# Performance work log

Hardware: AMD Instinct MI355X
Metric: run time of the kernel (lower is better)

The kernel has to match this reference:

```python
import jax, jax.numpy as jnp
import numpy as np

NEG_INF = -1e9  # finite mask value; exp underflows to exactly 0 in fp32


def setup_inputs() -> dict:
    key = jax.random.key(0)
    k1, k2 = jax.random.split(key)
    B, T, D = 16, 2048, 512
    x = jax.random.normal(k1, (B, T, D), dtype=jnp.float32)
    w = jax.random.normal(k2, (D, 1), dtype=jnp.float32) * (D ** -0.5)
    b = jnp.zeros((1,), dtype=jnp.float32)
    return {"x": x, "w": w, "b": b}


def reference(x, w, b):
    # x: [B,T,D]; Dense(1) scores shared across all output steps
    B, T, D = x.shape
    s = jnp.squeeze(x @ w, -1) + b[0]              # [B,T] per-position scalar score
    # output step t (t>=1) attends over strict prefix j < t.
    # row r = t-1 in [0, T-1): valid j <= r  -> lower-triangular mask [T-1, T]
    mask = jnp.tril(jnp.ones((T - 1, T), dtype=bool))
    logits = jnp.where(mask[None], s[:, None, :], NEG_INF)  # [B,T-1,T]
    attn = jax.nn.softmax(logits, axis=-1)                  # [B,T-1,T]
    ctx = jnp.einsum('brj,bjd->brd', attn, x)               # [B,T-1,D]
    # t == 0: passthrough of encoder output at step 0
    return jnp.concatenate([x[:, :1, :], ctx], axis=1)      # [B,T,D]
```

## Files before the change

### kernel.cpp

```cpp
#include <hip/hip_runtime.h>
#include <math.h>

#define B  16
#define T  2048
#define D  512
#define NS 64
#define L  (T / NS)
#define D4 (D / 4)

__device__ __forceinline__ void fma4(float4& a, float s, const float4& v) {
    a.x = fmaf(s, v.x, a.x); a.y = fmaf(s, v.y, a.y);
    a.z = fmaf(s, v.z, a.z); a.w = fmaf(s, v.w, a.w);
}

__global__ __launch_bounds__(256) void seg_kernel(const float* __restrict__ x,
                                                  const float* __restrict__ w,
                                                  const float* __restrict__ bias,
                                                  float* __restrict__ p_loc,
                                                  float* __restrict__ m_out,
                                                  float* __restrict__ q_out,
                                                  float* __restrict__ V) {
    int b = blockIdx.x / NS, k = blockIdx.x % NS;
    int t0 = k * L;
    int tid = threadIdx.x, lane = tid & 63, wv = tid >> 6;
    const float4* x4 = (const float4*)x + ((size_t)b * T + t0) * D4;
    const float4* w4 = (const float4*)w;
    float4 w0 = w4[lane], w1 = w4[lane + 64];

    float4 xr0[8], xr1[8];
    float dots[8];
#pragma unroll
    for (int r = 0; r < 8; ++r) {
        int j = wv * 8 + r;
        xr0[r] = x4[(size_t)j * D4 + lane];
        xr1[r] = x4[(size_t)j * D4 + lane + 64];
        dots[r] = xr0[r].x * w0.x + xr0[r].y * w0.y + xr0[r].z * w0.z + xr0[r].w * w0.w +
                  xr1[r].x * w1.x + xr1[r].y * w1.y + xr1[r].z * w1.z + xr1[r].w * w1.w;
    }

    __shared__ float s_sh[L], e_sh[L];
    __shared__ float accbuf[4][D];

#pragma unroll
    for (int r = 0; r < 8; ++r) {
        float d = dots[r];
#pragma unroll
        for (int off = 32; off > 0; off >>= 1) d += __shfl_xor(d, off);
        if (lane == 0) s_sh[wv * 8 + r] = d + bias[0];
    }
    __syncthreads();

    float mk = -1e30f;
#pragma unroll
    for (int j = 0; j < L; ++j) mk = fmaxf(mk, s_sh[j]);

    float4 a0 = {0.f, 0.f, 0.f, 0.f}, a1 = {0.f, 0.f, 0.f, 0.f};
#pragma unroll
    for (int r = 0; r < 8; ++r) {
        float e = __expf(s_sh[wv * 8 + r] - mk);
        if (lane == 0) e_sh[wv * 8 + r] = e;
        fma4(a0, e, xr0[r]); fma4(a1, e, xr1[r]);
    }
    ((float4*)accbuf[wv])[lane]      = a0;
    ((float4*)accbuf[wv])[lane + 64] = a1;
    __syncthreads();

    if (tid < 128) {
        float4 s0 = ((float4*)accbuf[0])[tid];
        float4 s1 = ((float4*)accbuf[1])[tid];
        float4 s2 = ((float4*)accbuf[2])[tid];
        float4 s3 = ((float4*)accbuf[3])[tid];
        float4 r;
        r.x = (s0.x + s1.x) + (s2.x + s3.x);
        r.y = (s0.y + s1.y) + (s2.y + s3.y);
        r.z = (s0.z + s1.z) + (s2.z + s3.z);
        r.w = (s0.w + s1.w) + (s2.w + s3.w);
        ((float4*)V)[((size_t)b * NS + k) * D4 + tid] = r;
    }
    if (tid < L) p_loc[(size_t)b * T + t0 + tid] = e_sh[tid];
    if (tid == 0) {
        m_out[b * NS + k] = mk;
        float q = 0.f;
#pragma unroll
        for (int j = 0; j < L; ++j) q += e_sh[j];
        q_out[b * NS + k] = q;
    }
}

__global__ __launch_bounds__(256) void out_kernel(const float* __restrict__ x,
                                                  const float* __restrict__ p_loc,
                                                  const float* __restrict__ m_g,
                                                  const float* __restrict__ q_g,
                                                  const float* __restrict__ V,
                                                  float* __restrict__ out) {
    const int blk = blockIdx.x;
    const int b = blk >> 6, k = blk & (NS - 1);
    const int t0 = k * L;
    const int tid = threadIdx.x, lane = tid & 63, wv = tid >> 6;

    const float4* x4 = (const float4*)x + ((size_t)b * T + t0) * D4;
    float4 xr0[8], xr1[8];
#pragma unroll
    for (int r = 0; r < 8; ++r) {
        const int j = wv * 8 + r;
        xr0[r] = x4[(size_t)j * D4 + lane];
        xr1[r] = x4[(size_t)j * D4 + lane + 64];
    }

    __shared__ float accbuf[4][D];
    __shared__ float sc_sh[NS];
    __shared__ float wl[L], il[L];

    const float m_i = m_g[b * NS + lane];
    const float q_i = q_g[b * NS + lane];
    float M = m_i;
#pragma unroll
    for (int off = 32; off > 0; off >>= 1) M = fmaxf(M, __shfl_xor(M, off));
    const float sc_i = __expf(m_i - M);
    const float qp = sc_i * q_i;
    float incl = qp;
#pragma unroll
    for (int off = 1; off < 64; off <<= 1) {
        const float t = __shfl_up(incl, off);
        if (lane >= off) incl += t;
    }
    const float Qexcl = __shfl(incl - qp, k);
    const float sck   = __shfl(sc_i, k);
    if (wv == 0) sc_sh[lane] = sc_i;
    __syncthreads();

    float4 s0 = {0.f, 0.f, 0.f, 0.f}, s1 = {0.f, 0.f, 0.f, 0.f};
    for (int kp = wv; kp < k; kp += 4) {
        const float sc = sc_sh[kp];
        const float4* Vp = (const float4*)V + ((size_t)b * NS + kp) * D4;
        fma4(s0, sc, Vp[lane]);
        fma4(s1, sc, Vp[lane + 64]);
    }
    ((float4*)accbuf[wv])[lane]      = s0;
    ((float4*)accbuf[wv])[lane + 64] = s1;

    if (wv == 0) {
        const float e_j = (lane < L) ? p_loc[(size_t)b * T + t0 + lane] : 0.f;
        float ce = e_j;
#pragma unroll
        for (int off = 1; off < 32; off <<= 1) {
            const float t = __shfl_up(ce, off);
            if (lane >= off) ce += t;
        }
        if (lane < L) {
            wl[lane] = sck * e_j;
            il[lane] = 1.0f / fmaf(sck, ce, Qexcl);
        }
    }
    __syncthreads();

    float4 seed0, seed1;
    {
        const float4 c0 = ((float4*)accbuf[0])[lane];
        const float4 c1 = ((float4*)accbuf[1])[lane];
        const float4 c2 = ((float4*)accbuf[2])[lane];
        const float4 c3 = ((float4*)accbuf[3])[lane];
        seed0.x = (c0.x + c1.x) + (c2.x + c3.x);
        seed0.y = (c0.y + c1.y) + (c2.y + c3.y);
        seed0.z = (c0.z + c1.z) + (c2.z + c3.z);
        seed0.w = (c0.w + c1.w) + (c2.w + c3.w);
        const float4 d0 = ((float4*)accbuf[0])[lane + 64];
        const float4 d1 = ((float4*)accbuf[1])[lane + 64];
        const float4 d2 = ((float4*)accbuf[2])[lane + 64];
        const float4 d3 = ((float4*)accbuf[3])[lane + 64];
        seed1.x = (d0.x + d1.x) + (d2.x + d3.x);
        seed1.y = (d0.y + d1.y) + (d2.y + d3.y);
        seed1.z = (d0.z + d1.z) + (d2.z + d3.z);
        seed1.w = (d0.w + d1.w) + (d2.w + d3.w);
    }

    float wcr[8], ilr[8];
    float4 t0v = {0.f, 0.f, 0.f, 0.f}, t1v = {0.f, 0.f, 0.f, 0.f};
#pragma unroll
    for (int r = 0; r < 8; ++r) {
        wcr[r] = wl[wv * 8 + r];
        ilr[r] = il[wv * 8 + r];
        fma4(t0v, wcr[r], xr0[r]); fma4(t1v, wcr[r], xr1[r]);
    }
    __syncthreads();
    ((float4*)accbuf[wv])[lane]      = t0v;
    ((float4*)accbuf[wv])[lane + 64] = t1v;
    __syncthreads();

    float4 p0 = seed0, p1 = seed1;
    for (int w2 = 0; w2 < wv; ++w2) {
        const float4 c0 = ((float4*)accbuf[w2])[lane];
        const float4 c1 = ((float4*)accbuf[w2])[lane + 64];
        p0.x += c0.x; p0.y += c0.y; p0.z += c0.z; p0.w += c0.w;
        p1.x += c1.x; p1.y += c1.y; p1.z += c1.z; p1.w += c1.w;
    }

    float4* outb = (float4*)out + (size_t)b * T * D4;
    if (k == 0 && wv == 0) {
        outb[lane]      = xr0[0];
        outb[lane + 64] = xr1[0];
    }
#pragma unroll
    for (int r = 0; r < 8; ++r) {
        fma4(p0, wcr[r], xr0[r]); fma4(p1, wcr[r], xr1[r]);
        const int t = t0 + wv * 8 + r;
        if (t < T - 1) {
            const float idn = ilr[r];
            float4 o0, o1;
            o0.x = p0.x * idn; o0.y = p0.y * idn; o0.z = p0.z * idn; o0.w = p0.w * idn;
            o1.x = p1.x * idn; o1.y = p1.y * idn; o1.z = p1.z * idn; o1.w = p1.w * idn;
            outb[(size_t)(t + 1) * D4 + lane]      = o0;
            outb[(size_t)(t + 1) * D4 + lane + 64] = o1;
        }
    }
}

extern "C" void kernel_launch(void* const* d_in, const int* in_sizes, int n_in,
                              void* d_out, int out_size, void* d_ws, size_t ws_size,
                              hipStream_t stream) {
    const float* x    = (const float*)d_in[0];
    const float* w    = (const float*)d_in[1];
    const float* bias = (const float*)d_in[2];
    float* out = (float*)d_out;

    float* p_loc = (float*)d_ws;
    float* m     = p_loc + (size_t)B * T;
    float* q     = m     + (size_t)B * NS;
    float* V     = q     + (size_t)B * NS;

    seg_kernel<<<B * NS, 256, 0, stream>>>(x, w, bias, p_loc, m, q, V);
    out_kernel<<<B * NS, 256, 0, stream>>>(x, p_loc, m, q, V, out);
}
```

Measured before the change: 41.06 us.

## Fuse segment and output kernels into single-pass decoupled-lookback kernel

Merges the two kernels into one. Each block takes a virtual block id from an atomic counter, publishes its segment max, sum and weighted vector V, then spin-waits on per-segment flags of earlier segments in the same batch before computing its outputs. This removes the second launch, the second read of x, and the p_loc round trip through global memory. In exchange it adds a memset, atomic spin-waits with a serial dependency chain across segments, and a 4-blocks-per-CU launch bound.

After: 110.1 us. 2.68x slower.

```diff
diff --git a/kernel.cpp b/kernel.cpp
--- a/kernel.cpp
+++ b/kernel.cpp
@@ -13,25 +13,30 @@
     a.z = fmaf(s, v.z, a.z); a.w = fmaf(s, v.w, a.w);
 }
 
-__global__ __launch_bounds__(256) void seg_kernel(const float* __restrict__ x,
-                                                  const float* __restrict__ w,
-                                                  const float* __restrict__ bias,
-                                                  float* __restrict__ p_loc,
-                                                  float* __restrict__ m_out,
-                                                  float* __restrict__ q_out,
-                                                  float* __restrict__ V) {
-    int b = blockIdx.x / NS, k = blockIdx.x % NS;
-    int t0 = k * L;
-    int tid = threadIdx.x, lane = tid & 63, wv = tid >> 6;
+__global__ __launch_bounds__(256, 4) void fused_lookback(
+        const float* __restrict__ x, const float* __restrict__ w,
+        const float* __restrict__ bias,
+        int* __restrict__ counter, int* __restrict__ flags,
+        float* __restrict__ m_g, float* __restrict__ q_g,
+        float* __restrict__ V, float* __restrict__ out) {
+    const int tid = threadIdx.x, lane = tid & 63, wv = tid >> 6;
+
+    __shared__ int vb_sh;
+    if (tid == 0) vb_sh = atomicAdd(counter, 1);
+    __syncthreads();
+    const int blk = vb_sh;
+    const int b = blk >> 6, k = blk & (NS - 1);
+    const int t0 = k * L;
+
     const float4* x4 = (const float4*)x + ((size_t)b * T + t0) * D4;
     const float4* w4 = (const float4*)w;
-    float4 w0 = w4[lane], w1 = w4[lane + 64];
+    const float4 w0 = w4[lane], w1 = w4[lane + 64];
 
     float4 xr0[8], xr1[8];
     float dots[8];
 #pragma unroll
     for (int r = 0; r < 8; ++r) {
-        int j = wv * 8 + r;
+        const int j = wv * 8 + r;
         xr0[r] = x4[(size_t)j * D4 + lane];
         xr1[r] = x4[(size_t)j * D4 + lane + 64];
         dots[r] = xr0[r].x * w0.x + xr0[r].y * w0.y + xr0[r].z * w0.z + xr0[r].w * w0.w +
@@ -40,6 +45,8 @@
 
     __shared__ float s_sh[L], e_sh[L];
     __shared__ float accbuf[4][D];
+    __shared__ float sc_sh[NS];
+    __shared__ float wl[L], il[L];
 
 #pragma unroll
     for (int r = 0; r < 8; ++r) {
@@ -57,7 +64,7 @@
     float4 a0 = {0.f, 0.f, 0.f, 0.f}, a1 = {0.f, 0.f, 0.f, 0.f};
 #pragma unroll
     for (int r = 0; r < 8; ++r) {
-        float e = __expf(s_sh[wv * 8 + r] - mk);
+        const float e = __expf(s_sh[wv * 8 + r] - mk);
         if (lane == 0) e_sh[wv * 8 + r] = e;
         fma4(a0, e, xr0[r]); fma4(a1, e, xr1[r]);
     }
@@ -66,67 +73,60 @@
     __syncthreads();
 
     if (tid < 128) {
-        float4 s0 = ((float4*)accbuf[0])[tid];
-        float4 s1 = ((float4*)accbuf[1])[tid];
-        float4 s2 = ((float4*)accbuf[2])[tid];
-        float4 s3 = ((float4*)accbuf[3])[tid];
-        float4 r;
-        r.x = (s0.x + s1.x) + (s2.x + s3.x);
-        r.y = (s0.y + s1.y) + (s2.y + s3.y);
-        r.z = (s0.z + s1.z) + (s2.z + s3.z);
-        r.w = (s0.w + s1.w) + (s2.w + s3.w);
-        ((float4*)V)[((size_t)b * NS + k) * D4 + tid] = r;
-    }
-    if (tid < L) p_loc[(size_t)b * T + t0 + tid] = e_sh[tid];
+        const float4 r0 = ((float4*)accbuf[0])[tid];
+        const float4 r1 = ((float4*)accbuf[1])[tid];
+        const float4 r2 = ((float4*)accbuf[2])[tid];
+        const float4 r3 = ((float4*)accbuf[3])[tid];
+        float4 rr;
+        rr.x = (r0.x + r1.x) + (r2.x + r3.x);
+        rr.y = (r0.y + r1.y) + (r2.y + r3.y);
+        rr.z = (r0.z + r1.z) + (r2.z + r3.z);
+        rr.w = (r0.w + r1.w) + (r2.w + r3.w);
+        ((float4*)V)[(size_t)blk * D4 + tid] = rr;
+    }
     if (tid == 0) {
-        m_out[b * NS + k] = mk;
+        m_g[blk] = mk;
         float q = 0.f;
 #pragma unroll
         for (int j = 0; j < L; ++j) q += e_sh[j];
-        q_out[b * NS + k] = q;
-    }
-}
-
-__global__ __launch_bounds__(256) void out_kernel(const float* __restrict__ x,
-                                                  const float* __restrict__ p_loc,
-                                                  const float* __restrict__ m_g,
-                                                  const float* __restrict__ q_g,
-                                                  const float* __restrict__ V,
-                                                  float* __restrict__ out) {
-    const int blk = blockIdx.x;
-    const int b = blk >> 6, k = blk & (NS - 1);
-    const int t0 = k * L;
-    const int tid = threadIdx.x, lane = tid & 63, wv = tid >> 6;
-
-    const float4* x4 = (const float4*)x + ((size_t)b * T + t0) * D4;
-    float4 xr0[8], xr1[8];
-#pragma unroll
-    for (int r = 0; r < 8; ++r) {
-        const int j = wv * 8 + r;
-        xr0[r] = x4[(size_t)j * D4 + lane];
-        xr1[r] = x4[(size_t)j * D4 + lane + 64];
-    }
-
-    __shared__ float accbuf[4][D];
-    __shared__ float sc_sh[NS];
-    __shared__ float wl[L], il[L];
-
-    const float m_i = m_g[b * NS + lane];
-    const float q_i = q_g[b * NS + lane];
-    float M = m_i;
-#pragma unroll
-    for (int off = 32; off > 0; off >>= 1) M = fmaxf(M, __shfl_xor(M, off));
-    const float sc_i = __expf(m_i - M);
-    const float qp = sc_i * q_i;
-    float incl = qp;
-#pragma unroll
-    for (int off = 1; off < 64; off <<= 1) {
-        const float t = __shfl_up(incl, off);
-        if (lane >= off) incl += t;
-    }
-    const float Qexcl = __shfl(incl - qp, k);
-    const float sck   = __shfl(sc_i, k);
-    if (wv == 0) sc_sh[lane] = sc_i;
+        q_g[blk] = q;
+    }
+    __syncthreads();
+    if (tid == 0) {
+        __threadfence();
+        __hip_atomic_store(&flags[blk], 1, __ATOMIC_RELEASE, __HIP_MEMORY_SCOPE_AGENT);
+    }
+
+    if (wv == 0) {
+        float mj = -1e30f, qj = 0.f;
+        if (lane < k) {
+            while (__hip_atomic_load(&flags[b * NS + lane], __ATOMIC_ACQUIRE,
+                                     __HIP_MEMORY_SCOPE_AGENT) == 0)
+                __builtin_amdgcn_s_sleep(2);
+            mj = m_g[b * NS + lane];
+            qj = q_g[b * NS + lane];
+        }
+        float REF = fmaxf(mk, mj);
+#pragma unroll
+        for (int off = 32; off > 0; off >>= 1) REF = fmaxf(REF, __shfl_xor(REF, off));
+        const float scj = (lane < k) ? __expf(mj - REF) : 0.f;
+        sc_sh[lane] = scj;
+        float qp = scj * qj;
+#pragma unroll
+        for (int off = 32; off > 0; off >>= 1) qp += __shfl_xor(qp, off);
+        const float sck = __expf(mk - REF);
+        const float e_j = (lane < L) ? e_sh[lane] : 0.f;
+        float ce = e_j;
+#pragma unroll
+        for (int off = 1; off < 32; off <<= 1) {
+            const float t = __shfl_up(ce, off);
+            if (lane >= off) ce += t;
+        }
+        if (lane < L) {
+            wl[lane] = sck * e_j;
+            il[lane] = 1.0f / fmaf(sck, ce, qp);
+        }
+    }
     __syncthreads();
 
     float4 s0 = {0.f, 0.f, 0.f, 0.f}, s1 = {0.f, 0.f, 0.f, 0.f};
@@ -138,20 +138,6 @@
     }
     ((float4*)accbuf[wv])[lane]      = s0;
     ((float4*)accbuf[wv])[lane + 64] = s1;
-
-    if (wv == 0) {
-        const float e_j = (lane < L) ? p_loc[(size_t)b * T + t0 + lane] : 0.f;
-        float ce = e_j;
-#pragma unroll
-        for (int off = 1; off < 32; off <<= 1) {
-            const float t = __shfl_up(ce, off);
-            if (lane >= off) ce += t;
-        }
-        if (lane < L) {
-            wl[lane] = sck * e_j;
-            il[lane] = 1.0f / fmaf(sck, ce, Qexcl);
-        }
-    }
     __syncthreads();
 
     float4 seed0, seed1;
@@ -223,11 +209,13 @@
     const float* bias = (const float*)d_in[2];
     float* out = (float*)d_out;
 
-    float* p_loc = (float*)d_ws;
-    float* m     = p_loc + (size_t)B * T;
-    float* q     = m     + (size_t)B * NS;
-    float* V     = q     + (size_t)B * NS;
-
-    seg_kernel<<<B * NS, 256, 0, stream>>>(x, w, bias, p_loc, m, q, V);
-    out_kernel<<<B * NS, 256, 0, stream>>>(x, p_loc, m, q, V, out);
+    int*   counter = (int*)d_ws;
+    int*   flags   = counter + 64;
+    float* m_g     = (float*)((char*)d_ws + 8192);
+    float* q_g     = m_g + (size_t)B * NS;
+    float* V       = q_g + (size_t)B * NS;
+
+    hipMemsetAsync(d_ws, 0, 8192, stream);
+    fused_lookback<<<B * NS, 256, 0, stream>>>(x, w, bias, counter, flags,
+                                               m_g, q_g, V, out);
 }
```

## Write unnormalized local prefix in first kernel, rescale output in second

Applied to the files above, without the earlier changes.

Moves the intra-segment prefix accumulation over x into the first kernel, which now writes unnormalized partial outputs directly to out along with local cumulative denominators. The second kernel no longer reads x; instead it reads back out, adds the cross-segment seed and rescales. This removes the re-read of x and the per-row FMAs in the second pass, but adds a full extra write and read of the output buffer.

After: 49.19 us. 19.8% more time.

```diff
diff --git a/kernel.cpp b/kernel.cpp
--- a/kernel.cpp
+++ b/kernel.cpp
@@ -5,33 +5,33 @@
 #define T  2048
 #define D  512
 #define NS 64
-#define L  (T / NS)
-#define D4 (D / 4)
+#define L  32
+#define D4 128
 
 __device__ __forceinline__ void fma4(float4& a, float s, const float4& v) {
     a.x = fmaf(s, v.x, a.x); a.y = fmaf(s, v.y, a.y);
     a.z = fmaf(s, v.z, a.z); a.w = fmaf(s, v.w, a.w);
 }
 
-__global__ __launch_bounds__(256) void seg_kernel(const float* __restrict__ x,
-                                                  const float* __restrict__ w,
-                                                  const float* __restrict__ bias,
-                                                  float* __restrict__ p_loc,
-                                                  float* __restrict__ m_out,
-                                                  float* __restrict__ q_out,
-                                                  float* __restrict__ V) {
-    int b = blockIdx.x / NS, k = blockIdx.x % NS;
-    int t0 = k * L;
-    int tid = threadIdx.x, lane = tid & 63, wv = tid >> 6;
+__global__ __launch_bounds__(256) void seg_scan_kernel(
+        const float* __restrict__ x, const float* __restrict__ w,
+        const float* __restrict__ bias,
+        float* __restrict__ m_g, float* __restrict__ q_g,
+        float* __restrict__ V, float* __restrict__ denloc,
+        float* __restrict__ out) {
+    const int b = blockIdx.x >> 6, k = blockIdx.x & (NS - 1);
+    const int t0 = k * L;
+    const int tid = threadIdx.x, lane = tid & 63, wv = tid >> 6;
+
     const float4* x4 = (const float4*)x + ((size_t)b * T + t0) * D4;
     const float4* w4 = (const float4*)w;
-    float4 w0 = w4[lane], w1 = w4[lane + 64];
+    const float4 w0 = w4[lane], w1 = w4[lane + 64];
 
     float4 xr0[8], xr1[8];
     float dots[8];
 #pragma unroll
     for (int r = 0; r < 8; ++r) {
-        int j = wv * 8 + r;
+        const int j = wv * 8 + r;
         xr0[r] = x4[(size_t)j * D4 + lane];
         xr1[r] = x4[(size_t)j * D4 + lane + 64];
         dots[r] = xr0[r].x * w0.x + xr0[r].y * w0.y + xr0[r].z * w0.z + xr0[r].w * w0.w +
@@ -54,62 +54,94 @@
 #pragma unroll
     for (int j = 0; j < L; ++j) mk = fmaxf(mk, s_sh[j]);
 
-    float4 a0 = {0.f, 0.f, 0.f, 0.f}, a1 = {0.f, 0.f, 0.f, 0.f};
-#pragma unroll
-    for (int r = 0; r < 8; ++r) {
-        float e = __expf(s_sh[wv * 8 + r] - mk);
-        if (lane == 0) e_sh[wv * 8 + r] = e;
-        fma4(a0, e, xr0[r]); fma4(a1, e, xr1[r]);
-    }
-    ((float4*)accbuf[wv])[lane]      = a0;
-    ((float4*)accbuf[wv])[lane + 64] = a1;
+    if (wv == 0) {
+        const float e = (lane < L) ? __expf(s_sh[lane] - mk) : 0.f;
+        if (lane < L) e_sh[lane] = e;
+        float q = e;
+#pragma unroll
+        for (int off = 32; off > 0; off >>= 1) q += __shfl_xor(q, off);
+        float ce = e;
+#pragma unroll
+        for (int off = 1; off < 32; off <<= 1) {
+            const float t = __shfl_up(ce, off);
+            if (lane >= off) ce += t;
+        }
+        if (lane < L) denloc[(size_t)b * T + t0 + lane] = ce;
+        if (lane == 0) { m_g[b * NS + k] = mk; q_g[b * NS + k] = q; }
+    }
+    __syncthreads();
+
+    float er[8];
+    float4 t0v = {0.f, 0.f, 0.f, 0.f}, t1v = {0.f, 0.f, 0.f, 0.f};
+#pragma unroll
+    for (int r = 0; r < 8; ++r) {
+        er[r] = e_sh[wv * 8 + r];
+        fma4(t0v, er[r], xr0[r]); fma4(t1v, er[r], xr1[r]);
+    }
+    ((float4*)accbuf[wv])[lane]      = t0v;
+    ((float4*)accbuf[wv])[lane + 64] = t1v;
     __syncthreads();
 
     if (tid < 128) {
-        float4 s0 = ((float4*)accbuf[0])[tid];
-        float4 s1 = ((float4*)accbuf[1])[tid];
-        float4 s2 = ((float4*)accbuf[2])[tid];
-        float4 s3 = ((float4*)accbuf[3])[tid];
-        float4 r;
-        r.x = (s0.x + s1.x) + (s2.x + s3.x);
-        r.y = (s0.y + s1.y) + (s2.y + s3.y);
-        r.z = (s0.z + s1.z) + (s2.z + s3.z);
-        r.w = (s0.w + s1.w) + (s2.w + s3.w);
-        ((float4*)V)[((size_t)b * NS + k) * D4 + tid] = r;
-    }
-    if (tid < L) p_loc[(size_t)b * T + t0 + tid] = e_sh[tid];
-    if (tid == 0) {
-        m_out[b * NS + k] = mk;
-        float q = 0.f;
-#pragma unroll
-        for (int j = 0; j < L; ++j) q += e_sh[j];
-        q_out[b * NS + k] = q;
-    }
-}
-
-__global__ __launch_bounds__(256) void out_kernel(const float* __restrict__ x,
-                                                  const float* __restrict__ p_loc,
-                                                  const float* __restrict__ m_g,
-                                                  const float* __restrict__ q_g,
-                                                  const float* __restrict__ V,
-                                                  float* __restrict__ out) {
-    const int blk = blockIdx.x;
-    const int b = blk >> 6, k = blk & (NS - 1);
+        const float4 r0 = ((float4*)accbuf[0])[tid];
+        const float4 r1 = ((float4*)accbuf[1])[tid];
+        const float4 r2 = ((float4*)accbuf[2])[tid];
+        const float4 r3 = ((float4*)accbuf[3])[tid];
+        float4 rr;
+        rr.x = (r0.x + r1.x) + (r2.x + r3.x);
+        rr.y = (r0.y + r1.y) + (r2.y + r3.y);
+        rr.z = (r0.z + r1.z) + (r2.z + r3.z);
+        rr.w = (r0.w + r1.w) + (r2.w + r3.w);
+        ((float4*)V)[((size_t)b * NS + k) * D4 + tid] = rr;
+    }
+
+    float4 p0 = {0.f, 0.f, 0.f, 0.f}, p1 = {0.f, 0.f, 0.f, 0.f};
+    for (int w2 = 0; w2 < wv; ++w2) {
+        const float4 c0 = ((float4*)accbuf[w2])[lane];
+        const float4 c1 = ((float4*)accbuf[w2])[lane + 64];
+        p0.x += c0.x; p0.y += c0.y; p0.z += c0.z; p0.w += c0.w;
+        p1.x += c1.x; p1.y += c1.y; p1.z += c1.z; p1.w += c1.w;
+    }
+
+    float4* outb = (float4*)out + (size_t)b * T * D4;
+    if (k == 0 && wv == 0) {
+        outb[lane]      = xr0[0];
+        outb[lane + 64] = xr1[0];
+    }
+#pragma unroll
+    for (int r = 0; r < 8; ++r) {
+        fma4(p0, er[r], xr0[r]); fma4(p1, er[r], xr1[r]);
+        const int t = t0 + wv * 8 + r;
+        if (t < T - 1) {
+            outb[(size_t)(t + 1) * D4 + lane]      = p0;
+            outb[(size_t)(t + 1) * D4 + lane + 64] = p1;
+        }
+    }
+}
+
+__global__ __launch_bounds__(256) void rescale_kernel(
+        const float* __restrict__ m_g, const float* __restrict__ q_g,
+        const float* __restrict__ V, const float* __restrict__ denloc,
+        float* __restrict__ out) {
+    const int b = blockIdx.x >> 6, k = blockIdx.x & (NS - 1);
     const int t0 = k * L;
     const int tid = threadIdx.x, lane = tid & 63, wv = tid >> 6;
 
-    const float4* x4 = (const float4*)x + ((size_t)b * T + t0) * D4;
-    float4 xr0[8], xr1[8];
-#pragma unroll
-    for (int r = 0; r < 8; ++r) {
-        const int j = wv * 8 + r;
-        xr0[r] = x4[(size_t)j * D4 + lane];
-        xr1[r] = x4[(size_t)j * D4 + lane + 64];
+    float4* outb = (float4*)out + (size_t)b * T * D4;
+
+    float4 c0[8], c1[8];
+#pragma unroll
+    for (int r = 0; r < 8; ++r) {
+        const int t = t0 + wv * 8 + r;
+        if (t < T - 1) {
+            c0[r] = outb[(size_t)(t + 1) * D4 + lane];
+            c1[r] = outb[(size_t)(t + 1) * D4 + lane + 64];
+        }
     }
 
     __shared__ float accbuf[4][D];
     __shared__ float sc_sh[NS];
-    __shared__ float wl[L], il[L];
+    __shared__ float il[L];
 
     const float m_i = m_g[b * NS + lane];
     const float q_i = q_g[b * NS + lane];
@@ -130,40 +162,30 @@
     __syncthreads();
 
     float4 s0 = {0.f, 0.f, 0.f, 0.f}, s1 = {0.f, 0.f, 0.f, 0.f};
+    const float4* Vb = (const float4*)V + (size_t)(b * NS) * D4;
     for (int kp = wv; kp < k; kp += 4) {
         const float sc = sc_sh[kp];
-        const float4* Vp = (const float4*)V + ((size_t)b * NS + kp) * D4;
-        fma4(s0, sc, Vp[lane]);
-        fma4(s1, sc, Vp[lane + 64]);
+        fma4(s0, sc, Vb[(size_t)kp * D4 + lane]);
+        fma4(s1, sc, Vb[(size_t)kp * D4 + lane + 64]);
     }
     ((float4*)accbuf[wv])[lane]      = s0;
     ((float4*)accbuf[wv])[lane + 64] = s1;
 
-    if (wv == 0) {
-        const float e_j = (lane < L) ? p_loc[(size_t)b * T + t0 + lane] : 0.f;
-        float ce = e_j;
-#pragma unroll
-        for (int off = 1; off < 32; off <<= 1) {
-            const float t = __shfl_up(ce, off);
-            if (lane >= off) ce += t;
-        }
-        if (lane < L) {
-            wl[lane] = sck * e_j;
-            il[lane] = 1.0f / fmaf(sck, ce, Qexcl);
-        }
+    if (wv == 0 && lane < L) {
+        il[lane] = 1.0f / fmaf(sck, denloc[(size_t)b * T + t0 + lane], Qexcl);
     }
     __syncthreads();
 
     float4 seed0, seed1;
     {
-        const float4 c0 = ((float4*)accbuf[0])[lane];
-        const float4 c1 = ((float4*)accbuf[1])[lane];
-        const float4 c2 = ((float4*)accbuf[2])[lane];
-        const float4 c3 = ((float4*)accbuf[3])[lane];
-        seed0.x = (c0.x + c1.x) + (c2.x + c3.x);
-        seed0.y = (c0.y + c1.y) + (c2.y + c3.y);
-        seed0.z = (c0.z + c1.z) + (c2.z + c3.z);
-        seed0.w = (c0.w + c1.w) + (c2.w + c3.w);
+        const float4 a0 = ((float4*)accbuf[0])[lane];
+        const float4 a1 = ((float4*)accbuf[1])[lane];
+        const float4 a2 = ((float4*)accbuf[2])[lane];
+        const float4 a3 = ((float4*)accbuf[3])[lane];
+        seed0.x = (a0.x + a1.x) + (a2.x + a3.x);
+        seed0.y = (a0.y + a1.y) + (a2.y + a3.y);
+        seed0.z = (a0.z + a1.z) + (a2.z + a3.z);
+        seed0.w = (a0.w + a1.w) + (a2.w + a3.w);
         const float4 d0 = ((float4*)accbuf[0])[lane + 64];
         const float4 d1 = ((float4*)accbuf[1])[lane + 64];
         const float4 d2 = ((float4*)accbuf[2])[lane + 64];
@@ -174,41 +196,21 @@
         seed1.w = (d0.w + d1.w) + (d2.w + d3.w);
     }
 
-    float wcr[8], ilr[8];
-    float4 t0v = {0.f, 0.f, 0.f, 0.f}, t1v = {0.f, 0.f, 0.f, 0.f};
-#pragma unroll
-    for (int r = 0; r < 8; ++r) {
-        wcr[r] = wl[wv * 8 + r];
-        ilr[r] = il[wv * 8 + r];
-        fma4(t0v, wcr[r], xr0[r]); fma4(t1v, wcr[r], xr1[r]);
-    }
-    __syncthreads();
-    ((float4*)accbuf[wv])[lane]      = t0v;
-    ((float4*)accbuf[wv])[lane + 64] = t1v;
-    __syncthreads();
-
-    float4 p0 = seed0, p1 = seed1;
-    for (int w2 = 0; w2 < wv; ++w2) {
-        const float4 c0 = ((float4*)accbuf[w2])[lane];
-        const float4 c1 = ((float4*)accbuf[w2])[lane + 64];
-        p0.x += c0.x; p0.y += c0.y; p0.z += c0.z; p0.w += c0.w;
-        p1.x += c1.x; p1.y += c1.y; p1.z += c1.z; p1.w += c1.w;
-    }
-
-    float4* outb = (float4*)out + (size_t)b * T * D4;
-    if (k == 0 && wv == 0) {
-        outb[lane]      = xr0[0];
-        outb[lane + 64] = xr1[0];
-    }
-#pragma unroll
-    for (int r = 0; r < 8; ++r) {
-        fma4(p0, wcr[r], xr0[r]); fma4(p1, wcr[r], xr1[r]);
-        const int t = t0 + wv * 8 + r;
+#pragma unroll
+    for (int r = 0; r < 8; ++r) {
+        const int jj = wv * 8 + r;
+        const int t = t0 + jj;
         if (t < T - 1) {
-            const float idn = ilr[r];
+            const float idn = il[jj];
             float4 o0, o1;
-            o0.x = p0.x * idn; o0.y = p0.y * idn; o0.z = p0.z * idn; o0.w = p0.w * idn;
-            o1.x = p1.x * idn; o1.y = p1.y * idn; o1.z = p1.z * idn; o1.w = p1.w * idn;
+            o0.x = fmaf(sck, c0[r].x, seed0.x) * idn;
+            o0.y = fmaf(sck, c0[r].y, seed0.y) * idn;
+            o0.z = fmaf(sck, c0[r].z, seed0.z) * idn;
+            o0.w = fmaf(sck, c0[r].w, seed0.w) * idn;
+            o1.x = fmaf(sck, c1[r].x, seed1.x) * idn;
+            o1.y = fmaf(sck, c1[r].y, seed1.y) * idn;
+            o1.z = fmaf(sck, c1[r].z, seed1.z) * idn;
+            o1.w = fmaf(sck, c1[r].w, seed1.w) * idn;
             outb[(size_t)(t + 1) * D4 + lane]      = o0;
             outb[(size_t)(t + 1) * D4 + lane + 64] = o1;
         }
@@ -223,11 +225,11 @@
     const float* bias = (const float*)d_in[2];
     float* out = (float*)d_out;
 
-    float* p_loc = (float*)d_ws;
-    float* m     = p_loc + (size_t)B * T;
-    float* q     = m     + (size_t)B * NS;
-    float* V     = q     + (size_t)B * NS;
-
-    seg_kernel<<<B * NS, 256, 0, stream>>>(x, w, bias, p_loc, m, q, V);
-    out_kernel<<<B * NS, 256, 0, stream>>>(x, p_loc, m, q, V, out);
-}
+    float* m_g    = (float*)d_ws;
+    float* q_g    = m_g    + (size_t)B * NS;
+    float* denloc = q_g    + (size_t)B * NS;
+    float* V      = denloc + (size_t)B * T;
+
+    seg_scan_kernel<<<B * NS, 256, 0, stream>>>(x, w, bias, m_g, q_g, V, denloc, out);
+    rescale_kernel <<<B * NS, 256, 0, stream>>>(m_g, q_g, V, denloc, out);
+}
```
